# Performance work log

Measured on AMD Instinct MI355X. Metric: run time of the kernel, lower is better.

Reference implementation:

```python
import jax, jax.numpy as jnp
import numpy as np

N = 100_000   # nodes per type
E = 800_000   # edges per relation
H = 128       # hidden_channels
O = 64        # out_channels
TIME_SCALE = 1.0
LN_EPS = 1e-5


def setup_inputs() -> dict:
    key = jax.random.key(0)
    ks = jax.random.split(key, 24)
    nrm = lambda k, shp, s=1.0: jax.random.normal(k, shp, jnp.float32) * s
    inp = {}
    inp["x_A"] = nrm(ks[0], (N, H))
    inp["x_B"] = nrm(ks[1], (N, H))
    inp["x_C"] = nrm(ks[2], (N, H))
    inp["t_A"] = jax.random.uniform(ks[3], (N,), jnp.float32) * 1000.0
    inp["t_B"] = jax.random.uniform(ks[4], (N,), jnp.float32) * 1000.0
    inp["t_C"] = jax.random.uniform(ks[5], (N,), jnp.float32) * 1000.0
    inp["edge1"] = jnp.stack([jax.random.randint(ks[6], (E,), 0, N),
                              jax.random.randint(ks[7], (E,), 0, N)]).astype(jnp.int32)
    inp["edge2"] = jnp.stack([jax.random.randint(ks[8], (E,), 0, N),
                              jax.random.randint(ks[9], (E,), 0, N)]).astype(jnp.int32)
    kk = 10
    for i in range(2):
        inp[f"Wl{i}"] = nrm(ks[kk], (H, H), 0.05); kk += 1
        inp[f"bl{i}"] = jnp.zeros((H,), jnp.float32)
        inp[f"W0{i}"] = nrm(ks[kk], (H, H), 0.05); kk += 1
        inp[f"b0{i}"] = jnp.zeros((H,), jnp.float32)
        inp[f"W1{i}"] = nrm(ks[kk], (H, H), 0.05); kk += 1
        inp[f"b1{i}"] = jnp.zeros((H,), jnp.float32)
        inp[f"gate{i}"] = jnp.asarray(0.5, jnp.float32)
        inp[f"lam{i}"] = jnp.asarray(0.1, jnp.float32)  # raw lambda
        inp[f"lng{i}"] = jnp.ones((H,), jnp.float32)
        inp[f"lnb{i}"] = jnp.zeros((H,), jnp.float32)
    inp["Wout"] = nrm(ks[kk], (H, O), 0.05)
    inp["bout"] = jnp.zeros((O,), jnp.float32)
    return inp


def _layer(h_src, h_dst, x0_dst, edge, t_src, t_dst,
           Wl, bl, W0, b0, W1, b1, gate, raw_lam, lng, lnb):
    s, d = edge[0], edge[1]
    n_dst = h_dst.shape[0]
    # per-edge time-decay weight
    lam = jax.nn.softplus(raw_lam) + 1e-8
    delta = jnp.maximum((t_dst[d] - t_src[s]) / TIME_SCALE, 0.0)
    w = jnp.exp(jnp.maximum(-lam * delta, -60.0))          # [E]
    # gather + weight + scatter-add  (propagate with aggr='add')
    msg = h_src[s] * w[:, None]                            # [E,H]
    agg = jax.ops.segment_sum(msg, d, num_segments=n_dst)  # [n_dst,H]
    deg = jnp.maximum(jax.ops.segment_sum(w, d, num_segments=n_dst), 1e-6)
    out = agg / deg[:, None]
    g = jax.nn.sigmoid(gate)
    y = out @ Wl + bl + (1.0 - g) * (h_dst @ W0 + b0) + g * (x0_dst @ W1 + b1)
    y = jax.nn.relu(y)
    mu = jnp.mean(y, axis=-1, keepdims=True)
    var = jnp.mean((y - mu) ** 2, axis=-1, keepdims=True)
    y = (y - mu) * jax.lax.rsqrt(var + LN_EPS) * lng + lnb
    # index_copy_: only nodes that appear as a destination get updated
    cnt = jax.ops.segment_sum(jnp.ones_like(w), d, num_segments=n_dst)
    return jnp.where((cnt > 0)[:, None], y, h_dst)


def reference(x_A, x_B, x_C, t_A, t_B, t_C, edge1, edge2,
              Wl0, bl0, W00, b00, W10, b10, gate0, lam0, lng0, lnb0,
              Wl1, bl1, W01, b01, W11, b11, gate1, lam1, lng1, lnb1,
              Wout, bout):
    # reversed(metapath): process (B,r2,C) with conv_idx=1 first, then (A,r1,B) with conv_idx=0
    h_C = _layer(x_B, x_C, x_C, edge2, t_B, t_C,
                 Wl1, bl1, W01, b01, W11, b11, gate1, lam1, lng1, lnb1)
    h_B = _layer(x_A, x_B, x_B, edge1, t_A, t_B,
                 Wl0, bl0, W00, b00, W10, b10, gate0, lam0, lng0, lnb0)
    del h_B  # target type is metapath[-1][2] == 'C'; B's update does not feed C
    return h_C @ Wout + bout
```

## Files before the change

kernel.cpp:

```cpp
#include <hip/hip_runtime.h>


#define HD 128
#define OD 64
#define SCAN_E 1024

typedef unsigned short u16;
typedef short v8s __attribute__((ext_vector_type(8)));
typedef float v4f __attribute__((ext_vector_type(4)));

union Frag {
    unsigned int u[4];
    uint4 q;
    v8s v;
};

__device__ __forceinline__ float softplus_f(float x) {
    return fmaxf(x, 0.0f) + log1pf(expf(-fabsf(x)));
}
__device__ __forceinline__ float sigmoid_f(float x) {
    return 1.0f / (1.0f + expf(-x));
}
__device__ __forceinline__ int swz(int r, int c) {
    int g = (c >> 2) ^ (r & 7);
    return r * 128 + g * 4 + (c & 3);
}

__device__ __forceinline__ void split_store(float x, u16* ph, u16* pl) {
    unsigned int b = __float_as_uint(x);
    unsigned int h = b & 0xffff0000u;
    *ph = (u16)(h >> 16);
    float r = x - __uint_as_float(h);
    *pl = (u16)(__float_as_uint(r) >> 16);
}

__device__ __forceinline__ void cvt_split8(const float* f, unsigned int* hi,
                                           unsigned int* lo) {
#pragma unroll
    for (int j = 0; j < 4; ++j) {
        unsigned int b0 = __float_as_uint(f[2 * j]);
        unsigned int b1 = __float_as_uint(f[2 * j + 1]);
        unsigned int h0 = b0 & 0xffff0000u;
        unsigned int h1 = b1 & 0xffff0000u;
        hi[j] = (h0 >> 16) | h1;
        float r0 = f[2 * j]     - __uint_as_float(h0);
        float r1 = f[2 * j + 1] - __uint_as_float(h1);
        lo[j] = (__float_as_uint(r0) >> 16) | (__float_as_uint(r1) & 0xffff0000u);
    }
}

__global__ __launch_bounds__(256) void k_prep(
    const int* __restrict__ edge, int* __restrict__ cnt, int E, int gE,
    const float* __restrict__ Wl, const float* __restrict__ W0,
    const float* __restrict__ W1, const float* __restrict__ Wout,
    const float* __restrict__ bl, const float* __restrict__ b0,
    const float* __restrict__ b1, const float* __restrict__ gatep,
    u16* __restrict__ wlh, u16* __restrict__ wll,
    u16* __restrict__ wch, u16* __restrict__ wcl,
    u16* __restrict__ woh, u16* __restrict__ wol, float* __restrict__ bc)
{
    if (blockIdx.x < (unsigned)gE) {
        int e = blockIdx.x * 256 + threadIdx.x;
        if (e < E) atomicAdd(cnt + edge[E + e], 1);
        return;
    }
    int i = (blockIdx.x - gE) * 256 + threadIdx.x;
    const float g = sigmoid_f(gatep[0]);
    if (i < 16384) {
        int n = i >> 7, k = i & 127;
        float a  = Wl[k * 128 + n];
        float w0 = W0[k * 128 + n];
        float w1 = W1[k * 128 + n];
        float c  = (1.f - g) * w0 + g * w1;
        int off = ((k >> 5) * 128 + n) * 32 + (k & 31);
        split_store(a, wlh + off, wll + off);
        split_store(c, wch + off, wcl + off);
    } else if (i < 24576) {
        int j = i - 16384;
        int n = j >> 7, k = j & 127;
        float v = Wout[k * 64 + n];
        int off = ((k >> 5) * 64 + n) * 32 + (k & 31);
        split_store(v, woh + off, wol + off);
    } else if (i < 24704) {
        int t = i - 24576;
        bc[t] = bl[t] + (1.f - g) * b0[t] + g * b1[t];
    }
}

__global__ __launch_bounds__(256) void k_scan1(
    const int* __restrict__ cnt, int* __restrict__ offs,
    int* __restrict__ part, int* __restrict__ tot, int N)
{
    __shared__ int sh[256];
    const int t = threadIdx.x;
    const int base = blockIdx.x * SCAN_E + t * 4;
    int v[4], sum = 0;
#pragma unroll
    for (int i = 0; i < 4; ++i) {
        int idx = base + i;
        v[i] = (idx < N) ? cnt[idx] : 0;
        sum += v[i];
    }
    sh[t] = sum;
    __syncthreads();
    for (int off = 1; off < 256; off <<= 1) {
        int x = (t >= off) ? sh[t - off] : 0;
        __syncthreads();
        sh[t] += x;
        __syncthreads();
    }
    int run = (t > 0) ? sh[t - 1] : 0;
    if (t == 255) part[blockIdx.x] = atomicAdd(tot, sh[255]);
#pragma unroll
    for (int i = 0; i < 4; ++i) {
        int idx = base + i;
        if (idx < N) offs[idx] = run;
        run += v[i];
    }
}

__global__ __launch_bounds__(256) void k_fillw(
    const int* __restrict__ edge, const float* __restrict__ tB,
    const float* __restrict__ tC, const float* __restrict__ lam_raw,
    const int* __restrict__ offs, const int* __restrict__ part,
    int* __restrict__ fillc, int2* __restrict__ srcw, int E)
{
    int e = blockIdx.x * 256 + threadIdx.x;
    if (e >= E) return;
    int s = edge[e];
    int d = edge[E + e];
    float lam = softplus_f(lam_raw[0]) + 1e-8f;
    float dt  = fmaxf(tC[d] - tB[s], 0.0f);
    float w   = expf(fmaxf(-lam * dt, -60.0f));
    int pos = offs[d] + part[d >> 10] + atomicAdd(fillc + d, 1);
    srcw[pos] = make_int2(s, __float_as_int(w));
}

__global__ __launch_bounds__(256) void k_gather(
    const float* __restrict__ xB, const int2* __restrict__ srcw,
    const int* __restrict__ offs, const int* __restrict__ part,
    const int* __restrict__ cnt, float* __restrict__ aggn, int N)
{
    const int wave = (blockIdx.x * 256 + threadIdx.x) >> 6;
    const int lane = threadIdx.x & 63;
    const int slot = lane >> 4;
    const int l4   = lane & 15;
    if (wave >= N) return;
    const int r    = wave;
    const int degc = cnt[r];

    float* dstp = aggn + (size_t)r * HD;
    if (degc == 0) {
        if (slot == 0) {
            *reinterpret_cast<float4*>(dstp + l4 * 4) = make_float4(0, 0, 0, 0);
            *reinterpret_cast<float4*>(dstp + 64 + l4 * 4) = make_float4(0, 0, 0, 0);
        }
        return;
    }

    const int start = offs[r] + part[r >> 10];
    float4 a0 = make_float4(0, 0, 0, 0), a1 = make_float4(0, 0, 0, 0);
    float sw = 0.f;
#pragma unroll 2
    for (int j = slot; j < degc; j += 4) {
        int2 swp = srcw[start + j];
        float w = __int_as_float(swp.y);
        const float* row = xB + (size_t)swp.x * HD;
        float4 x0 = *reinterpret_cast<const float4*>(row + l4 * 4);
        float4 x1 = *reinterpret_cast<const float4*>(row + 64 + l4 * 4);
        a0.x = fmaf(w, x0.x, a0.x); a0.y = fmaf(w, x0.y, a0.y);
        a0.z = fmaf(w, x0.z, a0.z); a0.w = fmaf(w, x0.w, a0.w);
        a1.x = fmaf(w, x1.x, a1.x); a1.y = fmaf(w, x1.y, a1.y);
        a1.z = fmaf(w, x1.z, a1.z); a1.w = fmaf(w, x1.w, a1.w);
        sw += w;
    }
#pragma unroll
    for (int m = 16; m <= 32; m <<= 1) {
        a0.x += __shfl_xor(a0.x, m); a0.y += __shfl_xor(a0.y, m);
        a0.z += __shfl_xor(a0.z, m); a0.w += __shfl_xor(a0.w, m);
        a1.x += __shfl_xor(a1.x, m); a1.y += __shfl_xor(a1.y, m);
        a1.z += __shfl_xor(a1.z, m); a1.w += __shfl_xor(a1.w, m);
        sw   += __shfl_xor(sw, m);
    }
    float inv = 1.0f / fmaxf(sw, 1e-6f);
    if (slot == 0) {
        a0.x *= inv; a0.y *= inv; a0.z *= inv; a0.w *= inv;
        a1.x *= inv; a1.y *= inv; a1.z *= inv; a1.w *= inv;
        *reinterpret_cast<float4*>(dstp + l4 * 4) = a0;
        *reinterpret_cast<float4*>(dstp + 64 + l4 * 4) = a1;
    }
}

__global__ __launch_bounds__(256) void k_fused(
    const float* __restrict__ xC, const float* __restrict__ aggn,
    const int* __restrict__ cnt,
    const u16* __restrict__ wlh, const u16* __restrict__ wll,
    const u16* __restrict__ wch, const u16* __restrict__ wcl,
    const u16* __restrict__ woh, const u16* __restrict__ wol,
    const float* __restrict__ bc, const float* __restrict__ lng,
    const float* __restrict__ lnb, const float* __restrict__ bout,
    float* __restrict__ out, int N)
{
    __shared__ float lds[4 * 16 * 128];

    const int lane = threadIdx.x & 63;
    const int wid  = threadIdx.x >> 6;
    const int lr   = lane & 15;
    const int kb   = lane >> 4;
    const int row0 = blockIdx.x * 64 + wid * 16;
    float* myl = lds + wid * 16 * 128;

    v4f acc[8] = {};

#pragma unroll
    for (int mat = 0; mat < 2; ++mat) {
        const float* Asrc = mat ? xC : aggn;
        const uint4* BH = (const uint4*)(mat ? wch : wlh);
        const uint4* BL = (const uint4*)(mat ? wcl : wll);
#pragma unroll
        for (int kc = 0; kc < 4; ++kc) {
            Frag ah, al;
            {
                int r = row0 + lr;
                r = (r < N) ? r : (N - 1);
                const float4* ap = (const float4*)(
                    Asrc + (size_t)r * HD + kc * 32 + kb * 8);
                float4 u0 = ap[0], u1 = ap[1];
                float f[8] = {u0.x, u0.y, u0.z, u0.w, u1.x, u1.y, u1.z, u1.w};
                cvt_split8(f, ah.u, al.u);
            }
#pragma unroll
            for (int ct = 0; ct < 8; ++ct) {
                int idx = kc * 512 + (ct * 16 + lr) * 4 + kb;
                Frag bh, bl;
                bh.q = BH[idx];
                bl.q = BL[idx];
                acc[ct] = __builtin_amdgcn_mfma_f32_16x16x32_bf16(
                    ah.v, bh.v, acc[ct], 0, 0, 0);
                acc[ct] = __builtin_amdgcn_mfma_f32_16x16x32_bf16(
                    ah.v, bl.v, acc[ct], 0, 0, 0);
                acc[ct] = __builtin_amdgcn_mfma_f32_16x16x32_bf16(
                    al.v, bh.v, acc[ct], 0, 0, 0);
            }
        }
    }

    float bcv[8], gav[8], bev[8];
#pragma unroll
    for (int ct = 0; ct < 8; ++ct) {
        int c = ct * 16 + lr;
        bcv[ct] = bc[c];
        gav[ct] = lng[c];
        bev[ct] = lnb[c];
    }

    {
        int rq = row0 + kb * 4;
        int cvr[4] = {0, 0, 0, 0};
        if (rq < N) {
            int4 cv = *(const int4*)(cnt + rq);
            cvr[0] = cv.x; cvr[1] = cv.y; cvr[2] = cv.z; cvr[3] = cv.w;
        }
#pragma unroll
        for (int reg = 0; reg < 4; ++reg) {
            int rloc = kb * 4 + reg;
            int r    = rq + reg;
            float yv[8];
            float s = 0.f, q = 0.f;
#pragma unroll
            for (int ct = 0; ct < 8; ++ct) {
                float v = acc[ct][reg] + bcv[ct];
                v = fmaxf(v, 0.0f);
                yv[ct] = v;
                s += v;
                q += v * v;
            }
#pragma unroll
            for (int m = 1; m < 16; m <<= 1) {
                s += __shfl_xor(s, m);
                q += __shfl_xor(q, m);
            }
            float mu   = s * (1.0f / 128.0f);
            float var  = q * (1.0f / 128.0f) - mu * mu;
            float rstd = rsqrtf(var + 1e-5f);

            if (r < N) {
                if (cvr[reg] > 0) {
#pragma unroll
                    for (int ct = 0; ct < 8; ++ct)
                        myl[swz(rloc, ct * 16 + lr)] =
                            (yv[ct] - mu) * rstd * gav[ct] + bev[ct];
                } else {
                    size_t base = (size_t)r * HD;
#pragma unroll
                    for (int ct = 0; ct < 8; ++ct)
                        myl[swz(rloc, ct * 16 + lr)] = xC[base + ct * 16 + lr];
                }
            } else {
#pragma unroll
                for (int ct = 0; ct < 8; ++ct)
                    myl[swz(rloc, ct * 16 + lr)] = 0.0f;
            }
        }
    }

    v4f acc2[4] = {};
    const uint4* BH3 = (const uint4*)woh;
    const uint4* BL3 = (const uint4*)wol;

#pragma unroll
    for (int kc = 0; kc < 4; ++kc) {
        Frag ah, al;
        {
            int c0 = kc * 32 + kb * 8;
            float4 u0 = *reinterpret_cast<const float4*>(&myl[swz(lr, c0)]);
            float4 u1 = *reinterpret_cast<const float4*>(&myl[swz(lr, c0 + 4)]);
            float f[8] = {u0.x, u0.y, u0.z, u0.w, u1.x, u1.y, u1.z, u1.w};
            cvt_split8(f, ah.u, al.u);
        }
#pragma unroll
        for (int ct = 0; ct < 4; ++ct) {
            int idx = kc * 256 + (ct * 16 + lr) * 4 + kb;
            Frag bh, bl;
            bh.q = BH3[idx];
            bl.q = BL3[idx];
            acc2[ct] = __builtin_amdgcn_mfma_f32_16x16x32_bf16(
                ah.v, bh.v, acc2[ct], 0, 0, 0);
            acc2[ct] = __builtin_amdgcn_mfma_f32_16x16x32_bf16(
                ah.v, bl.v, acc2[ct], 0, 0, 0);
            acc2[ct] = __builtin_amdgcn_mfma_f32_16x16x32_bf16(
                al.v, bh.v, acc2[ct], 0, 0, 0);
        }
    }

    float bov[4];
#pragma unroll
    for (int ct = 0; ct < 4; ++ct) bov[ct] = bout[ct * 16 + lr];

#pragma unroll
    for (int reg = 0; reg < 4; ++reg) {
        int r = row0 + kb * 4 + reg;
        if (r < N) {
#pragma unroll
            for (int ct = 0; ct < 4; ++ct)
                out[(size_t)r * OD + ct * 16 + lr] = acc2[ct][reg] + bov[ct];
        }
    }
}

extern "C" void kernel_launch(void* const* d_in, const int* in_sizes, int n_in,
                              void* d_out, int out_size, void* d_ws, size_t ws_size,
                              hipStream_t stream) {
    const float* xB    = (const float*)d_in[1];
    const float* xC    = (const float*)d_in[2];
    const float* tB    = (const float*)d_in[4];
    const float* tC    = (const float*)d_in[5];
    const int*   edge2 = (const int*)d_in[7];
    const float* Wl1   = (const float*)d_in[18];
    const float* bl1   = (const float*)d_in[19];
    const float* W01   = (const float*)d_in[20];
    const float* b01   = (const float*)d_in[21];
    const float* W11   = (const float*)d_in[22];
    const float* b11   = (const float*)d_in[23];
    const float* gate1 = (const float*)d_in[24];
    const float* lam1  = (const float*)d_in[25];
    const float* lng1  = (const float*)d_in[26];
    const float* lnb1  = (const float*)d_in[27];
    const float* Wout  = (const float*)d_in[28];
    const float* bout  = (const float*)d_in[29];

    const int N = in_sizes[2] / HD;
    const int E = in_sizes[7] / 2;

    int*   cnt   = (int*)d_ws;
    int*   fillc = cnt + N;
    int*   offs  = fillc + N;
    int*   part  = offs + N;
    int*   tot   = part + 128;
    int2*  srcw  = (int2*)(tot + 4);
    u16*   wlh   = (u16*)(srcw + E);
    u16*   wll   = wlh + 16384;
    u16*   wch   = wll + 16384;
    u16*   wcl   = wch + 16384;
    u16*   woh   = wcl + 16384;
    u16*   wol   = woh + 8192;
    float* bc    = (float*)(wol + 8192);
    float* buf   = bc + 128;

    hipMemsetAsync(cnt, 0, (size_t)2 * N * sizeof(int), stream);
    hipMemsetAsync(tot, 0, sizeof(int), stream);

    dim3 blk(256);
    const int gE = (E + 255) / 256;
    const int NB = (N + SCAN_E - 1) / SCAN_E;

    k_prep <<<gE + 97, blk, 0, stream>>>(edge2, cnt, E, gE,
                                         Wl1, W01, W11, Wout, bl1, b01, b11,
                                         gate1, wlh, wll, wch, wcl, woh, wol, bc);
    k_scan1<<<NB, blk, 0, stream>>>(cnt, offs, part, tot, N);
    k_fillw<<<gE, blk, 0, stream>>>(edge2, tB, tC, lam1, offs, part, fillc, srcw, E);

    const int gN64 = (N * 64 + 255) / 256;
    k_gather<<<gN64, blk, 0, stream>>>(xB, srcw, offs, part, cnt, buf, N);

    const int GB = (N + 63) / 64;
    k_fused<<<GB, blk, 0, stream>>>(xC, buf, cnt, wlh, wll, wch, wcl, woh, wol,
                                    bc, lng1, lnb1, bout, (float*)d_out, N);
}
```

Baseline: 240.6 us.

## Double-buffer A tiles via global_load_lds and give each wave 32 rows

Each wave in the fused dense kernel now handles 32 rows instead of 16. Every B-fragment load from the split-bf16 weights now feeds two row tiles, which halves weight-fragment traffic per row. A activation tiles are staged into LDS with asynchronous global_load_lds into a swizzled double buffer, so the next k-chunk loads while the current one runs through MFMAs. The cost is more accumulator registers (two 8-tile sets), which may lower occupancy, a vmcnt(0) wait every iteration, and half as many blocks.

```diff
diff --git a/kernel.cpp b/kernel.cpp
--- a/kernel.cpp
+++ b/kernel.cpp
@@ -24,6 +24,26 @@
 __device__ __forceinline__ int swz(int r, int c) {
     int g = (c >> 2) ^ (r & 7);
     return r * 128 + g * 4 + (c & 3);
+}
+
+__device__ __forceinline__ void gload_lds16(const float* g, float* l) {
+    __builtin_amdgcn_global_load_lds(
+        (const __attribute__((address_space(1))) void*)g,
+        (__attribute__((address_space(3))) void*)l, 16, 0, 0);
+}
+
+__device__ __forceinline__ void stage_kc(const float* __restrict__ Asrc, int kc,
+                                         float* bufp, int row0, int lane, int N) {
+#pragma unroll
+    for (int t = 0; t < 4; ++t) {
+        int rowL = t * 8 + (lane >> 3);
+        int gch  = lane & 7;
+        int rG   = row0 + rowL;
+        rG = (rG < N) ? rG : (N - 1);
+        const float* srcp = Asrc + (size_t)rG * HD + kc * 32 +
+                            ((gch ^ (rowL & 7)) << 2);
+        gload_lds16(srcp, bufp + t * 256);
+    }
 }
 
 __device__ __forceinline__ void split_store(float x, u16* ph, u16* pl) {
@@ -201,48 +221,61 @@
     const float* __restrict__ lnb, const float* __restrict__ bout,
     float* __restrict__ out, int N)
 {
-    __shared__ float lds[4 * 16 * 128];
+    __shared__ float lds[4 * 2048];
 
     const int lane = threadIdx.x & 63;
     const int wid  = threadIdx.x >> 6;
     const int lr   = lane & 15;
     const int kb   = lane >> 4;
-    const int row0 = blockIdx.x * 64 + wid * 16;
-    float* myl = lds + wid * 16 * 128;
-
-    v4f acc[8] = {};
-
-#pragma unroll
-    for (int mat = 0; mat < 2; ++mat) {
-        const float* Asrc = mat ? xC : aggn;
+    const int row0 = blockIdx.x * 128 + wid * 32;
+    float* myl = lds + wid * 2048;
+    float* st[2] = {myl, myl + 1024};
+
+    v4f acc[2][8] = {};
+    const float* As[2] = {aggn, xC};
+
+    stage_kc(As[0], 0, st[0], row0, lane, N);
+    int par = 0;
+#pragma unroll
+    for (int it = 0; it < 8; ++it) {
+        const int mat = it >> 2;
+        const int kc  = it & 3;
+        asm volatile("s_waitcnt vmcnt(0)" ::: "memory");
+        if (it < 7) {
+            int nit = it + 1;
+            stage_kc(As[nit >> 2], nit & 3, st[par ^ 1], row0, lane, N);
+        }
+        const float* cb = st[par];
+        Frag ah[2], al[2];
+#pragma unroll
+        for (int rt = 0; rt < 2; ++rt) {
+            int row = rt * 16 + lr;
+            float4 u0 = *reinterpret_cast<const float4*>(
+                cb + row * 32 + (((2 * kb)     ^ (row & 7)) << 2));
+            float4 u1 = *reinterpret_cast<const float4*>(
+                cb + row * 32 + (((2 * kb + 1) ^ (row & 7)) << 2));
+            float f[8] = {u0.x, u0.y, u0.z, u0.w, u1.x, u1.y, u1.z, u1.w};
+            cvt_split8(f, ah[rt].u, al[rt].u);
+        }
         const uint4* BH = (const uint4*)(mat ? wch : wlh);
         const uint4* BL = (const uint4*)(mat ? wcl : wll);
 #pragma unroll
-        for (int kc = 0; kc < 4; ++kc) {
-            Frag ah, al;
-            {
-                int r = row0 + lr;
-                r = (r < N) ? r : (N - 1);
-                const float4* ap = (const float4*)(
-                    Asrc + (size_t)r * HD + kc * 32 + kb * 8);
-                float4 u0 = ap[0], u1 = ap[1];
-                float f[8] = {u0.x, u0.y, u0.z, u0.w, u1.x, u1.y, u1.z, u1.w};
-                cvt_split8(f, ah.u, al.u);
-            }
-#pragma unroll
-            for (int ct = 0; ct < 8; ++ct) {
-                int idx = kc * 512 + (ct * 16 + lr) * 4 + kb;
-                Frag bh, bl;
-                bh.q = BH[idx];
-                bl.q = BL[idx];
-                acc[ct] = __builtin_amdgcn_mfma_f32_16x16x32_bf16(
-                    ah.v, bh.v, acc[ct], 0, 0, 0);
-                acc[ct] = __builtin_amdgcn_mfma_f32_16x16x32_bf16(
-                    ah.v, bl.v, acc[ct], 0, 0, 0);
-                acc[ct] = __builtin_amdgcn_mfma_f32_16x16x32_bf16(
-                    al.v, bh.v, acc[ct], 0, 0, 0);
-            }
-        }
+        for (int ct = 0; ct < 8; ++ct) {
+            int idx = kc * 512 + (ct * 16 + lr) * 4 + kb;
+            Frag bh, bl;
+            bh.q = BH[idx];
+            bl.q = BL[idx];
+#pragma unroll
+            for (int rt = 0; rt < 2; ++rt) {
+                acc[rt][ct] = __builtin_amdgcn_mfma_f32_16x16x32_bf16(
+                    ah[rt].v, bh.v, acc[rt][ct], 0, 0, 0);
+                acc[rt][ct] = __builtin_amdgcn_mfma_f32_16x16x32_bf16(
+                    ah[rt].v, bl.v, acc[rt][ct], 0, 0, 0);
+                acc[rt][ct] = __builtin_amdgcn_mfma_f32_16x16x32_bf16(
+                    al[rt].v, bh.v, acc[rt][ct], 0, 0, 0);
+            }
+        }
+        par ^= 1;
     }
 
     float bcv[8], gav[8], bev[8];
@@ -253,9 +286,16 @@
         gav[ct] = lng[c];
         bev[ct] = lnb[c];
     }
-
-    {
-        int rq = row0 + kb * 4;
+    float bov[4];
+#pragma unroll
+    for (int ct = 0; ct < 4; ++ct) bov[ct] = bout[ct * 16 + lr];
+
+    const uint4* BH3 = (const uint4*)woh;
+    const uint4* BL3 = (const uint4*)wol;
+
+#pragma unroll
+    for (int rt = 0; rt < 2; ++rt) {
+        int rq = row0 + rt * 16 + kb * 4;
         int cvr[4] = {0, 0, 0, 0};
         if (rq < N) {
             int4 cv = *(const int4*)(cnt + rq);
@@ -269,7 +309,7 @@
             float s = 0.f, q = 0.f;
 #pragma unroll
             for (int ct = 0; ct < 8; ++ct) {
-                float v = acc[ct][reg] + bcv[ct];
+                float v = acc[rt][ct][reg] + bcv[ct];
                 v = fmaxf(v, 0.0f);
                 yv[ct] = v;
                 s += v;
@@ -302,48 +342,41 @@
                     myl[swz(rloc, ct * 16 + lr)] = 0.0f;
             }
         }
-    }
-
-    v4f acc2[4] = {};
-    const uint4* BH3 = (const uint4*)woh;
-    const uint4* BL3 = (const uint4*)wol;
-
-#pragma unroll
-    for (int kc = 0; kc < 4; ++kc) {
-        Frag ah, al;
-        {
-            int c0 = kc * 32 + kb * 8;
-            float4 u0 = *reinterpret_cast<const float4*>(&myl[swz(lr, c0)]);
-            float4 u1 = *reinterpret_cast<const float4*>(&myl[swz(lr, c0 + 4)]);
-            float f[8] = {u0.x, u0.y, u0.z, u0.w, u1.x, u1.y, u1.z, u1.w};
-            cvt_split8(f, ah.u, al.u);
-        }
-#pragma unroll
-        for (int ct = 0; ct < 4; ++ct) {
-            int idx = kc * 256 + (ct * 16 + lr) * 4 + kb;
-            Frag bh, bl;
-            bh.q = BH3[idx];
-            bl.q = BL3[idx];
-            acc2[ct] = __builtin_amdgcn_mfma_f32_16x16x32_bf16(
-                ah.v, bh.v, acc2[ct], 0, 0, 0);
-            acc2[ct] = __builtin_amdgcn_mfma_f32_16x16x32_bf16(
-                ah.v, bl.v, acc2[ct], 0, 0, 0);
-            acc2[ct] = __builtin_amdgcn_mfma_f32_16x16x32_bf16(
-                al.v, bh.v, acc2[ct], 0, 0, 0);
-        }
-    }
-
-    float bov[4];
-#pragma unroll
-    for (int ct = 0; ct < 4; ++ct) bov[ct] = bout[ct * 16 + lr];
-
-#pragma unroll
-    for (int reg = 0; reg < 4; ++reg) {
-        int r = row0 + kb * 4 + reg;
-        if (r < N) {
-#pragma unroll
-            for (int ct = 0; ct < 4; ++ct)
-                out[(size_t)r * OD + ct * 16 + lr] = acc2[ct][reg] + bov[ct];
+
+        v4f acc2[4] = {};
+#pragma unroll
+        for (int kc = 0; kc < 4; ++kc) {
+            Frag ah, al;
+            {
+                int c0 = kc * 32 + kb * 8;
+                float4 u0 = *reinterpret_cast<const float4*>(&myl[swz(lr, c0)]);
+                float4 u1 = *reinterpret_cast<const float4*>(&myl[swz(lr, c0 + 4)]);
+                float f[8] = {u0.x, u0.y, u0.z, u0.w, u1.x, u1.y, u1.z, u1.w};
+                cvt_split8(f, ah.u, al.u);
+            }
+#pragma unroll
+            for (int ct = 0; ct < 4; ++ct) {
+                int idx = kc * 256 + (ct * 16 + lr) * 4 + kb;
+                Frag bh, bl;
+                bh.q = BH3[idx];
+                bl.q = BL3[idx];
+                acc2[ct] = __builtin_amdgcn_mfma_f32_16x16x32_bf16(
+                    ah.v, bh.v, acc2[ct], 0, 0, 0);
+                acc2[ct] = __builtin_amdgcn_mfma_f32_16x16x32_bf16(
+                    ah.v, bl.v, acc2[ct], 0, 0, 0);
+                acc2[ct] = __builtin_amdgcn_mfma_f32_16x16x32_bf16(
+                    al.v, bh.v, acc2[ct], 0, 0, 0);
+            }
+        }
+
+#pragma unroll
+        for (int reg = 0; reg < 4; ++reg) {
+            int r = rq + reg;
+            if (r < N) {
+#pragma unroll
+                for (int ct = 0; ct < 4; ++ct)
+                    out[(size_t)r * OD + ct * 16 + lr] = acc2[ct][reg] + bov[ct];
+            }
         }
     }
 }
@@ -403,7 +436,7 @@
     const int gN64 = (N * 64 + 255) / 256;
     k_gather<<<gN64, blk, 0, stream>>>(xB, srcw, offs, part, cnt, buf, N);
 
-    const int GB = (N + 63) / 64;
+    const int GB = (N + 127) / 128;
     k_fused<<<GB, blk, 0, stream>>>(xC, buf, cnt, wlh, wll, wch, wcl, woh, wol,
                                     bc, lng1, lnb1, bout, (float*)d_out, N);
 }
```

Result: faster. 227.5 us (-5.4%).

## Pre-split activations to bf16 hi/lo and retile fused GEMM across waves

Applied to the files above, without the earlier changes.

The gather kernel now writes its normalized aggregate as bf16 hi/lo halves, and the prep kernel gains blocks that pre-split xC the same way. The fused kernel processes 128 rows per block. It streams A tiles into LDS with global_load_lds, and each wave owns a 32-column slice of the output, so weight fragments are loaded once per k-chunk instead of per row tile. LayerNorm statistics are reduced across waves through LDS, and the output GEMM runs in four row groups. The aim is to avoid redundant weight loads and in-kernel fp32 conversion. The cost is more synchronisation, an extra pass over xC, and added workspace for the split copies.

```diff
diff --git a/kernel.cpp b/kernel.cpp
--- a/kernel.cpp
+++ b/kernel.cpp
@@ -13,6 +13,7 @@
     unsigned int u[4];
     uint4 q;
     v8s v;
+    u16 h[8];
 };
 
 __device__ __forceinline__ float softplus_f(float x) {
@@ -24,6 +25,12 @@
 __device__ __forceinline__ int swz(int r, int c) {
     int g = (c >> 2) ^ (r & 7);
     return r * 128 + g * 4 + (c & 3);
+}
+
+__device__ __forceinline__ void gload_lds16(const void* g, void* l) {
+    __builtin_amdgcn_global_load_lds(
+        (const __attribute__((address_space(1))) void*)g,
+        (__attribute__((address_space(3))) void*)l, 16, 0, 0);
 }
 
 __device__ __forceinline__ void split_store(float x, u16* ph, u16* pl) {
@@ -32,6 +39,17 @@
     *ph = (u16)(h >> 16);
     float r = x - __uint_as_float(h);
     *pl = (u16)(__float_as_uint(r) >> 16);
+}
+
+__device__ __forceinline__ void split_pack8(const float* f, Frag* hi, Frag* lo) {
+#pragma unroll
+    for (int j = 0; j < 8; ++j) {
+        unsigned int b = __float_as_uint(f[j]);
+        unsigned int h = b & 0xffff0000u;
+        hi->h[j] = (u16)(h >> 16);
+        float r = f[j] - __uint_as_float(h);
+        lo->h[j] = (u16)(__float_as_uint(r) >> 16);
+    }
 }
 
 __device__ __forceinline__ void cvt_split8(const float* f, unsigned int* hi,
@@ -55,35 +73,50 @@
     const float* __restrict__ W1, const float* __restrict__ Wout,
     const float* __restrict__ bl, const float* __restrict__ b0,
     const float* __restrict__ b1, const float* __restrict__ gatep,
+    const float* __restrict__ xC,
     u16* __restrict__ wlh, u16* __restrict__ wll,
     u16* __restrict__ wch, u16* __restrict__ wcl,
-    u16* __restrict__ woh, u16* __restrict__ wol, float* __restrict__ bc)
+    u16* __restrict__ woh, u16* __restrict__ wol, float* __restrict__ bc,
+    u16* __restrict__ xch, u16* __restrict__ xcl, int N)
 {
     if (blockIdx.x < (unsigned)gE) {
         int e = blockIdx.x * 256 + threadIdx.x;
         if (e < E) atomicAdd(cnt + edge[E + e], 1);
         return;
     }
-    int i = (blockIdx.x - gE) * 256 + threadIdx.x;
-    const float g = sigmoid_f(gatep[0]);
-    if (i < 16384) {
-        int n = i >> 7, k = i & 127;
-        float a  = Wl[k * 128 + n];
-        float w0 = W0[k * 128 + n];
-        float w1 = W1[k * 128 + n];
-        float c  = (1.f - g) * w0 + g * w1;
-        int off = ((k >> 5) * 128 + n) * 32 + (k & 31);
-        split_store(a, wlh + off, wll + off);
-        split_store(c, wch + off, wcl + off);
-    } else if (i < 24576) {
-        int j = i - 16384;
-        int n = j >> 7, k = j & 127;
-        float v = Wout[k * 64 + n];
-        int off = ((k >> 5) * 64 + n) * 32 + (k & 31);
-        split_store(v, woh + off, wol + off);
-    } else if (i < 24704) {
-        int t = i - 24576;
-        bc[t] = bl[t] + (1.f - g) * b0[t] + g * b1[t];
+    if (blockIdx.x < (unsigned)(gE + 97)) {
+        int i = (blockIdx.x - gE) * 256 + threadIdx.x;
+        const float g = sigmoid_f(gatep[0]);
+        if (i < 16384) {
+            int n = i >> 7, k = i & 127;
+            float a  = Wl[k * 128 + n];
+            float w0 = W0[k * 128 + n];
+            float w1 = W1[k * 128 + n];
+            float c  = (1.f - g) * w0 + g * w1;
+            int off = ((k >> 5) * 128 + n) * 32 + (k & 31);
+            split_store(a, wlh + off, wll + off);
+            split_store(c, wch + off, wcl + off);
+        } else if (i < 24576) {
+            int j = i - 16384;
+            int n = j >> 7, k = j & 127;
+            float v = Wout[k * 64 + n];
+            int off = ((k >> 5) * 64 + n) * 32 + (k & 31);
+            split_store(v, woh + off, wol + off);
+        } else if (i < 24704) {
+            int t = i - 24576;
+            bc[t] = bl[t] + (1.f - g) * b0[t] + g * b1[t];
+        }
+        return;
+    }
+    long long e8 = ((long long)(blockIdx.x - gE - 97) * 256 + threadIdx.x) * 8;
+    if (e8 < (long long)N * HD) {
+        float4 u0 = *reinterpret_cast<const float4*>(xC + e8);
+        float4 u1 = *reinterpret_cast<const float4*>(xC + e8 + 4);
+        float f[8] = {u0.x, u0.y, u0.z, u0.w, u1.x, u1.y, u1.z, u1.w};
+        Frag hi, lo;
+        split_pack8(f, &hi, &lo);
+        *reinterpret_cast<uint4*>(xch + e8) = hi.q;
+        *reinterpret_cast<uint4*>(xcl + e8) = lo.q;
     }
 }
 
@@ -139,7 +172,8 @@
 __global__ __launch_bounds__(256) void k_gather(
     const float* __restrict__ xB, const int2* __restrict__ srcw,
     const int* __restrict__ offs, const int* __restrict__ part,
-    const int* __restrict__ cnt, float* __restrict__ aggn, int N)
+    const int* __restrict__ cnt, u16* __restrict__ aggh,
+    u16* __restrict__ aggl, int N)
 {
     const int wave = (blockIdx.x * 256 + threadIdx.x) >> 6;
     const int lane = threadIdx.x & 63;
@@ -149,11 +183,11 @@
     const int r    = wave;
     const int degc = cnt[r];
 
-    float* dstp = aggn + (size_t)r * HD;
     if (degc == 0) {
         if (slot == 0) {
-            *reinterpret_cast<float4*>(dstp + l4 * 4) = make_float4(0, 0, 0, 0);
-            *reinterpret_cast<float4*>(dstp + 64 + l4 * 4) = make_float4(0, 0, 0, 0);
+            uint4 z = make_uint4(0, 0, 0, 0);
+            *reinterpret_cast<uint4*>(aggh + (size_t)r * HD + l4 * 8) = z;
+            *reinterpret_cast<uint4*>(aggl + (size_t)r * HD + l4 * 8) = z;
         }
         return;
     }
@@ -165,9 +199,9 @@
     for (int j = slot; j < degc; j += 4) {
         int2 swp = srcw[start + j];
         float w = __int_as_float(swp.y);
-        const float* row = xB + (size_t)swp.x * HD;
-        float4 x0 = *reinterpret_cast<const float4*>(row + l4 * 4);
-        float4 x1 = *reinterpret_cast<const float4*>(row + 64 + l4 * 4);
+        const float* row = xB + (size_t)swp.x * HD + l4 * 8;
+        float4 x0 = *reinterpret_cast<const float4*>(row);
+        float4 x1 = *reinterpret_cast<const float4*>(row + 4);
         a0.x = fmaf(w, x0.x, a0.x); a0.y = fmaf(w, x0.y, a0.y);
         a0.z = fmaf(w, x0.z, a0.z); a0.w = fmaf(w, x0.w, a0.w);
         a1.x = fmaf(w, x1.x, a1.x); a1.y = fmaf(w, x1.y, a1.y);
@@ -184,15 +218,18 @@
     }
     float inv = 1.0f / fmaxf(sw, 1e-6f);
     if (slot == 0) {
-        a0.x *= inv; a0.y *= inv; a0.z *= inv; a0.w *= inv;
-        a1.x *= inv; a1.y *= inv; a1.z *= inv; a1.w *= inv;
-        *reinterpret_cast<float4*>(dstp + l4 * 4) = a0;
-        *reinterpret_cast<float4*>(dstp + 64 + l4 * 4) = a1;
+        float f[8] = {a0.x * inv, a0.y * inv, a0.z * inv, a0.w * inv,
+                      a1.x * inv, a1.y * inv, a1.z * inv, a1.w * inv};
+        Frag hi, lo;
+        split_pack8(f, &hi, &lo);
+        *reinterpret_cast<uint4*>(aggh + (size_t)r * HD + l4 * 8) = hi.q;
+        *reinterpret_cast<uint4*>(aggl + (size_t)r * HD + l4 * 8) = lo.q;
     }
 }
 
 __global__ __launch_bounds__(256) void k_fused(
-    const float* __restrict__ xC, const float* __restrict__ aggn,
+    const u16* __restrict__ aggh, const u16* __restrict__ aggl,
+    const u16* __restrict__ xch, const u16* __restrict__ xcl,
     const int* __restrict__ cnt,
     const u16* __restrict__ wlh, const u16* __restrict__ wll,
     const u16* __restrict__ wch, const u16* __restrict__ wcl,
@@ -201,77 +238,85 @@
     const float* __restrict__ lnb, const float* __restrict__ bout,
     float* __restrict__ out, int N)
 {
-    __shared__ float lds[4 * 16 * 128];
-
-    const int lane = threadIdx.x & 63;
-    const int wid  = threadIdx.x >> 6;
+    __shared__ float sm[5120];
+    u16*   ab16 = (u16*)sm;
+    float2* pr  = (float2*)&sm[4096];
+    float* hc   = sm;
+
+    const int tid  = threadIdx.x;
+    const int lane = tid & 63;
+    const int wid  = tid >> 6;
     const int lr   = lane & 15;
     const int kb   = lane >> 4;
-    const int row0 = blockIdx.x * 64 + wid * 16;
-    float* myl = lds + wid * 16 * 128;
-
-    v4f acc[8] = {};
-
-#pragma unroll
-    for (int mat = 0; mat < 2; ++mat) {
-        const float* Asrc = mat ? xC : aggn;
+    const int row0 = blockIdx.x * 128;
+
+    const u16* Ah[2] = {aggh, xch};
+    const u16* Al[2] = {aggl, xcl};
+
+    v4f acc[8][2] = {};
+
+#pragma unroll
+    for (int ch = 0; ch < 8; ++ch) {
+        const int mat = ch >> 2, kc = ch & 3;
+#pragma unroll
+        for (int c = 0; c < 2; ++c) {
+            int rowL = c * 64 + (tid >> 2);
+            int g    = tid & 3;
+            int rG   = row0 + rowL;
+            rG = (rG < N) ? rG : (N - 1);
+            size_t so = (size_t)rG * HD + kc * 32 + g * 8;
+            gload_lds16(Ah[mat] + so, ab16 + c * 2048 + wid * 512);
+            gload_lds16(Al[mat] + so, ab16 + 4096 + c * 2048 + wid * 512);
+        }
+        __syncthreads();
+
+        Frag bh[2], bl[2];
         const uint4* BH = (const uint4*)(mat ? wch : wlh);
         const uint4* BL = (const uint4*)(mat ? wcl : wll);
 #pragma unroll
-        for (int kc = 0; kc < 4; ++kc) {
+        for (int ct = 0; ct < 2; ++ct) {
+            int n   = wid * 32 + ct * 16 + lr;
+            int idx = kc * 512 + n * 4 + kb;
+            bh[ct].q = BH[idx];
+            bl[ct].q = BL[idx];
+        }
+#pragma unroll
+        for (int rt = 0; rt < 8; ++rt) {
+            int ro = (rt * 16 + lr) * 32 + kb * 8;
             Frag ah, al;
-            {
-                int r = row0 + lr;
-                r = (r < N) ? r : (N - 1);
-                const float4* ap = (const float4*)(
-                    Asrc + (size_t)r * HD + kc * 32 + kb * 8);
-                float4 u0 = ap[0], u1 = ap[1];
-                float f[8] = {u0.x, u0.y, u0.z, u0.w, u1.x, u1.y, u1.z, u1.w};
-                cvt_split8(f, ah.u, al.u);
-            }
-#pragma unroll
-            for (int ct = 0; ct < 8; ++ct) {
-                int idx = kc * 512 + (ct * 16 + lr) * 4 + kb;
-                Frag bh, bl;
-                bh.q = BH[idx];
-                bl.q = BL[idx];
-                acc[ct] = __builtin_amdgcn_mfma_f32_16x16x32_bf16(
-                    ah.v, bh.v, acc[ct], 0, 0, 0);
-                acc[ct] = __builtin_amdgcn_mfma_f32_16x16x32_bf16(
-                    ah.v, bl.v, acc[ct], 0, 0, 0);
-                acc[ct] = __builtin_amdgcn_mfma_f32_16x16x32_bf16(
-                    al.v, bh.v, acc[ct], 0, 0, 0);
-            }
-        }
-    }
-
-    float bcv[8], gav[8], bev[8];
-#pragma unroll
-    for (int ct = 0; ct < 8; ++ct) {
-        int c = ct * 16 + lr;
+            ah.q = *reinterpret_cast<const uint4*>(ab16 + ro);
+            al.q = *reinterpret_cast<const uint4*>(ab16 + 4096 + ro);
+#pragma unroll
+            for (int ct = 0; ct < 2; ++ct) {
+                acc[rt][ct] = __builtin_amdgcn_mfma_f32_16x16x32_bf16(
+                    ah.v, bh[ct].v, acc[rt][ct], 0, 0, 0);
+                acc[rt][ct] = __builtin_amdgcn_mfma_f32_16x16x32_bf16(
+                    ah.v, bl[ct].v, acc[rt][ct], 0, 0, 0);
+                acc[rt][ct] = __builtin_amdgcn_mfma_f32_16x16x32_bf16(
+                    al.v, bh[ct].v, acc[rt][ct], 0, 0, 0);
+            }
+        }
+        __syncthreads();
+    }
+
+    float bcv[2], gav[2], bev[2];
+#pragma unroll
+    for (int ct = 0; ct < 2; ++ct) {
+        int c = wid * 32 + ct * 16 + lr;
         bcv[ct] = bc[c];
         gav[ct] = lng[c];
         bev[ct] = lnb[c];
     }
-
-    {
-        int rq = row0 + kb * 4;
-        int cvr[4] = {0, 0, 0, 0};
-        if (rq < N) {
-            int4 cv = *(const int4*)(cnt + rq);
-            cvr[0] = cv.x; cvr[1] = cv.y; cvr[2] = cv.z; cvr[3] = cv.w;
-        }
+    const float bov = bout[wid * 16 + lr];
+
+#pragma unroll
+    for (int rt = 0; rt < 8; ++rt) {
 #pragma unroll
         for (int reg = 0; reg < 4; ++reg) {
-            int rloc = kb * 4 + reg;
-            int r    = rq + reg;
-            float yv[8];
             float s = 0.f, q = 0.f;
 #pragma unroll
-            for (int ct = 0; ct < 8; ++ct) {
-                float v = acc[ct][reg] + bcv[ct];
-                v = fmaxf(v, 0.0f);
-                yv[ct] = v;
+            for (int ct = 0; ct < 2; ++ct) {
+                float v = fmaxf(acc[rt][ct][reg] + bcv[ct], 0.0f);
                 s += v;
                 q += v * v;
             }
@@ -280,71 +325,103 @@
                 s += __shfl_xor(s, m);
                 q += __shfl_xor(q, m);
             }
-            float mu   = s * (1.0f / 128.0f);
-            float var  = q * (1.0f / 128.0f) - mu * mu;
-            float rstd = rsqrtf(var + 1e-5f);
-
-            if (r < N) {
-                if (cvr[reg] > 0) {
-#pragma unroll
-                    for (int ct = 0; ct < 8; ++ct)
-                        myl[swz(rloc, ct * 16 + lr)] =
-                            (yv[ct] - mu) * rstd * gav[ct] + bev[ct];
-                } else {
-                    size_t base = (size_t)r * HD;
-#pragma unroll
-                    for (int ct = 0; ct < 8; ++ct)
-                        myl[swz(rloc, ct * 16 + lr)] = xC[base + ct * 16 + lr];
-                }
-            } else {
-#pragma unroll
-                for (int ct = 0; ct < 8; ++ct)
-                    myl[swz(rloc, ct * 16 + lr)] = 0.0f;
-            }
-        }
-    }
-
-    v4f acc2[4] = {};
+            if (lr == 0)
+                pr[(rt * 16 + kb * 4 + reg) * 4 + wid] = make_float2(s, q);
+        }
+    }
+    __syncthreads();
+    if (tid < 128) {
+        float s = 0.f, q = 0.f;
+#pragma unroll
+        for (int w = 0; w < 4; ++w) {
+            float2 p = pr[tid * 4 + w];
+            s += p.x;
+            q += p.y;
+        }
+        float mu  = s * (1.0f / 128.0f);
+        float var = q * (1.0f / 128.0f) - mu * mu;
+        pr[tid * 4] = make_float2(mu, rsqrtf(var + 1e-5f));
+    }
+    __syncthreads();
+
     const uint4* BH3 = (const uint4*)woh;
     const uint4* BL3 = (const uint4*)wol;
 
 #pragma unroll
-    for (int kc = 0; kc < 4; ++kc) {
-        Frag ah, al;
-        {
-            int c0 = kc * 32 + kb * 8;
-            float4 u0 = *reinterpret_cast<const float4*>(&myl[swz(lr, c0)]);
-            float4 u1 = *reinterpret_cast<const float4*>(&myl[swz(lr, c0 + 4)]);
-            float f[8] = {u0.x, u0.y, u0.z, u0.w, u1.x, u1.y, u1.z, u1.w};
-            cvt_split8(f, ah.u, al.u);
-        }
-#pragma unroll
-        for (int ct = 0; ct < 4; ++ct) {
-            int idx = kc * 256 + (ct * 16 + lr) * 4 + kb;
-            Frag bh, bl;
-            bh.q = BH3[idx];
-            bl.q = BL3[idx];
-            acc2[ct] = __builtin_amdgcn_mfma_f32_16x16x32_bf16(
-                ah.v, bh.v, acc2[ct], 0, 0, 0);
-            acc2[ct] = __builtin_amdgcn_mfma_f32_16x16x32_bf16(
-                ah.v, bl.v, acc2[ct], 0, 0, 0);
-            acc2[ct] = __builtin_amdgcn_mfma_f32_16x16x32_bf16(
-                al.v, bh.v, acc2[ct], 0, 0, 0);
-        }
-    }
-
-    float bov[4];
-#pragma unroll
-    for (int ct = 0; ct < 4; ++ct) bov[ct] = bout[ct * 16 + lr];
-
-#pragma unroll
-    for (int reg = 0; reg < 4; ++reg) {
-        int r = row0 + kb * 4 + reg;
-        if (r < N) {
-#pragma unroll
-            for (int ct = 0; ct < 4; ++ct)
-                out[(size_t)r * OD + ct * 16 + lr] = acc2[ct][reg] + bov[ct];
-        }
+    for (int rg = 0; rg < 4; ++rg) {
+#pragma unroll
+        for (int rt2 = 0; rt2 < 2; ++rt2) {
+            const int rt    = rg * 2 + rt2;
+            const int lrow0 = rt2 * 16 + kb * 4;
+            const int rq    = row0 + rg * 32 + lrow0;
+            int cvr[4] = {0, 0, 0, 0};
+            if (rq < N) {
+                int4 cv = *(const int4*)(cnt + rq);
+                cvr[0] = cv.x; cvr[1] = cv.y; cvr[2] = cv.z; cvr[3] = cv.w;
+            }
+#pragma unroll
+            for (int reg = 0; reg < 4; ++reg) {
+                const int lrow = lrow0 + reg;
+                const int r    = rq + reg;
+                float2 mr = pr[(rg * 32 + lrow) * 4];
+#pragma unroll
+                for (int ct = 0; ct < 2; ++ct) {
+                    int col = wid * 32 + ct * 16 + lr;
+                    float val = 0.0f;
+                    if (r < N) {
+                        if (cvr[reg] > 0) {
+                            float y = fmaxf(acc[rt][ct][reg] + bcv[ct], 0.0f);
+                            val = (y - mr.x) * mr.y * gav[ct] + bev[ct];
+                        } else {
+                            size_t xo = (size_t)r * HD + col;
+                            unsigned int hb = ((unsigned int)xch[xo]) << 16;
+                            unsigned int lb = ((unsigned int)xcl[xo]) << 16;
+                            val = __uint_as_float(hb) + __uint_as_float(lb);
+                        }
+                    }
+                    hc[swz(lrow, col)] = val;
+                }
+            }
+        }
+        __syncthreads();
+
+        v4f acc2[2] = {};
+#pragma unroll
+        for (int kcc = 0; kcc < 4; ++kcc) {
+            Frag b3h, b3l;
+            {
+                int n   = wid * 16 + lr;
+                int idx = kcc * 256 + n * 4 + kb;
+                b3h.q = BH3[idx];
+                b3l.q = BL3[idx];
+            }
+#pragma unroll
+            for (int rt3 = 0; rt3 < 2; ++rt3) {
+                int rr = rt3 * 16 + lr;
+                int c0 = kcc * 32 + kb * 8;
+                float4 u0 = *reinterpret_cast<const float4*>(&hc[swz(rr, c0)]);
+                float4 u1 = *reinterpret_cast<const float4*>(&hc[swz(rr, c0 + 4)]);
+                float f[8] = {u0.x, u0.y, u0.z, u0.w, u1.x, u1.y, u1.z, u1.w};
+                Frag ah, al;
+                cvt_split8(f, ah.u, al.u);
+                acc2[rt3] = __builtin_amdgcn_mfma_f32_16x16x32_bf16(
+                    ah.v, b3h.v, acc2[rt3], 0, 0, 0);
+                acc2[rt3] = __builtin_amdgcn_mfma_f32_16x16x32_bf16(
+                    ah.v, b3l.v, acc2[rt3], 0, 0, 0);
+                acc2[rt3] = __builtin_amdgcn_mfma_f32_16x16x32_bf16(
+                    al.v, b3h.v, acc2[rt3], 0, 0, 0);
+            }
+        }
+#pragma unroll
+        for (int rt3 = 0; rt3 < 2; ++rt3) {
+#pragma unroll
+            for (int reg = 0; reg < 4; ++reg) {
+                int r = row0 + rg * 32 + rt3 * 16 + kb * 4 + reg;
+                if (r < N)
+                    out[(size_t)r * OD + wid * 16 + lr] = acc2[rt3][reg] + bov;
+            }
+        }
+        __syncthreads();
     }
 }
 
@@ -385,7 +462,10 @@
     u16*   woh   = wcl + 16384;
     u16*   wol   = woh + 8192;
     float* bc    = (float*)(wol + 8192);
-    float* buf   = bc + 128;
+    u16*   aggh  = (u16*)(bc + 128);
+    u16*   aggl  = aggh + (size_t)N * HD;
+    u16*   xch   = aggl + (size_t)N * HD;
+    u16*   xcl   = xch + (size_t)N * HD;
 
     hipMemsetAsync(cnt, 0, (size_t)2 * N * sizeof(int), stream);
     hipMemsetAsync(tot, 0, sizeof(int), stream);
@@ -393,17 +473,20 @@
     dim3 blk(256);
     const int gE = (E + 255) / 256;
     const int NB = (N + SCAN_E - 1) / SCAN_E;
-
-    k_prep <<<gE + 97, blk, 0, stream>>>(edge2, cnt, E, gE,
-                                         Wl1, W01, W11, Wout, bl1, b01, b11,
-                                         gate1, wlh, wll, wch, wcl, woh, wol, bc);
+    const int gX = (N * (HD / 8) + 255) / 256;
+
+    k_prep <<<gE + 97 + gX, blk, 0, stream>>>(edge2, cnt, E, gE,
+                                              Wl1, W01, W11, Wout, bl1, b01, b11,
+                                              gate1, xC, wlh, wll, wch, wcl,
+                                              woh, wol, bc, xch, xcl, N);
     k_scan1<<<NB, blk, 0, stream>>>(cnt, offs, part, tot, N);
     k_fillw<<<gE, blk, 0, stream>>>(edge2, tB, tC, lam1, offs, part, fillc, srcw, E);
 
     const int gN64 = (N * 64 + 255) / 256;
-    k_gather<<<gN64, blk, 0, stream>>>(xB, srcw, offs, part, cnt, buf, N);
-
-    const int GB = (N + 63) / 64;
-    k_fused<<<GB, blk, 0, stream>>>(xC, buf, cnt, wlh, wll, wch, wcl, woh, wol,
+    k_gather<<<gN64, blk, 0, stream>>>(xB, srcw, offs, part, cnt, aggh, aggl, N);
+
+    const int GB = (N + 127) / 128;
+    k_fused<<<GB, blk, 0, stream>>>(aggh, aggl, xch, xcl, cnt,
+                                    wlh, wll, wch, wcl, woh, wol,
                                     bc, lng1, lnb1, bout, (float*)d_out, N);
 }
```

After: 280.2 us. 1.16x slower.
